# Optimization experiments

Hardware: AMD Instinct MI355X
Metric: run time of the kernel (lower is better)

The kernel has to match this reference:

```python
import jax, jax.numpy as jnp
import numpy as np

IN_CH, OUT_CH, MODES = 64, 64, 16
BATCH, N = 64, 8192


def setup_inputs() -> dict:
    key = jax.random.key(0)
    k1, k2, k3 = jax.random.split(key, 3)
    scale = 1.0 / (IN_CH * OUT_CH)
    x = jax.random.normal(k1, (BATCH, IN_CH, N), dtype=jnp.float32)
    w_real = scale * jax.random.uniform(k2, (IN_CH, OUT_CH, MODES), dtype=jnp.float32)
    w_imag = scale * jax.random.uniform(k3, (IN_CH, OUT_CH, MODES), dtype=jnp.float32)
    return {"x": x, "w_real": w_real, "w_imag": w_imag}


def reference(x, w_real, w_imag):
    # x: (b, in_ch, n) real. weights: (in_ch, out_ch, modes) complex.
    n = x.shape[-1]
    weights = w_real + 1j * w_imag                      # complex64
    x_ft = jnp.fft.rfft(x)                              # (b, in_ch, n//2+1) complex
    # multiply only the lowest `modes` frequencies by learned complex weights
    out_modes = jnp.einsum('bix,iox->box', x_ft[:, :, :MODES], weights)
    n_freq = n // 2 + 1
    out_ft = jnp.zeros((x.shape[0], OUT_CH, n_freq), dtype=jnp.complex64)
    out_ft = out_ft.at[:, :, :MODES].set(out_modes)
    return jnp.fft.irfft(out_ft, n=n)                   # (b, out_ch, n) real
```

## Files before the change

kernel.cpp:

```cpp
#include <hip/hip_runtime.h>

#define NPTS 8192

typedef __bf16 bf16x8 __attribute__((ext_vector_type(8)));
typedef short short8 __attribute__((ext_vector_type(8)));
typedef float f32x4 __attribute__((ext_vector_type(4)));


__device__ __forceinline__ void split8(const float* v, short8& h, short8& l) {
#pragma unroll
    for (int j = 0; j < 8; ++j) {
        unsigned u = __float_as_uint(v[j]);
        h[j] = (short)(u >> 16);
        float lo = v[j] - __uint_as_float(u & 0xffff0000u);
        unsigned ul = __float_as_uint(lo);
        l[j] = (short)((ul + 0x7fffu + ((ul >> 16) & 1u)) >> 16);
    }
}

__global__ __launch_bounds__(256) void prep_kernel(const float* __restrict__ wr,
                                                   const float* __restrict__ wi,
                                                   float* __restrict__ wtr,
                                                   float* __restrict__ wti,
                                                   ushort* __restrict__ bas) {
    const int bid = blockIdx.x, t = threadIdx.x;
    if (bid < 256) {
        int idx = bid * 256 + t;
        int i = idx >> 10, o = (idx >> 4) & 63, k = idx & 15;
        int dst = k * 4096 + i * 64 + o;
        wtr[dst] = wr[idx];
        wti[dst] = wi[idx];
    } else {
        int e = (bid - 256) * 256 + t;
        int j = e & 7;
        int lane = (e >> 3) & 63;
        int gk = (e >> 9) & 255;
        int ct = e >> 17;
        int m = lane & 15;
        int n = gk * 32 + ((lane >> 4) & 3) * 8 + j;
        int p = (m * n) & 8191;
        float a = (float)p * (1.0f / 4096.0f);
        float v = ct ? -sinpif(a) : cospif(a);
        unsigned u = __float_as_uint(v);
        unsigned hb = (u + 0x7fffu + ((u >> 16) & 1u)) >> 16;
        float hf = __uint_as_float(hb << 16);
        float lo = v - hf;
        unsigned ul = __float_as_uint(lo);
        unsigned lb = (ul + 0x7fffu + ((ul >> 16) & 1u)) >> 16;
        bas[e] = (ushort)hb;
        bas[262144 + e] = (ushort)lb;
    }
}

__global__ __launch_bounds__(256) void dft_kernel(const float* __restrict__ x,
                                                  const ushort* __restrict__ bas,
                                                  float* __restrict__ Xp) {
    const int t = threadIdx.x;
    const int lane = t & 63, w = t >> 6;
    const int rb = blockIdx.x >> 4, seg = blockIdx.x & 15;
    const int rowq = lane >> 4;
    const int row = rb * 64 + w * 16 + (lane & 15);
    const float* xp = x + (size_t)row * NPTS + seg * 512 + rowq * 8;
    const bf16x8* bh = (const bf16x8*)bas;
    const bf16x8* bl = (const bf16x8*)(bas + 262144);
    const int gk0 = seg * 16;

    f32x4 acc0 = {0.f, 0.f, 0.f, 0.f};
    f32x4 acc1 = {0.f, 0.f, 0.f, 0.f};

    float4 xa = *(const float4*)xp;
    float4 xb = *(const float4*)(xp + 4);
    bf16x8 c0h = bh[gk0 * 64 + lane];
    bf16x8 c1h = bh[(256 + gk0) * 64 + lane];
    bf16x8 c0l = bl[gk0 * 64 + lane];
    bf16x8 c1l = bl[(256 + gk0) * 64 + lane];

    for (int ks = 0; ks < 16; ++ks) {
        float v[8] = {xa.x, xa.y, xa.z, xa.w, xb.x, xb.y, xb.z, xb.w};
        short8 hsv, lsv;
        split8(v, hsv, lsv);
        bf16x8 ah = __builtin_bit_cast(bf16x8, hsv);
        bf16x8 al = __builtin_bit_cast(bf16x8, lsv);

        float4 nxa, nxb;
        bf16x8 n0h, n1h, n0l, n1l;
        if (ks < 15) {
            const float* xq = xp + (ks + 1) * 32;
            nxa = *(const float4*)xq;
            nxb = *(const float4*)(xq + 4);
            int gk = gk0 + ks + 1;
            n0h = bh[gk * 64 + lane];
            n1h = bh[(256 + gk) * 64 + lane];
            n0l = bl[gk * 64 + lane];
            n1l = bl[(256 + gk) * 64 + lane];
        }

        acc0 = __builtin_amdgcn_mfma_f32_16x16x32_bf16(ah, c0h, acc0, 0, 0, 0);
        acc1 = __builtin_amdgcn_mfma_f32_16x16x32_bf16(ah, c1h, acc1, 0, 0, 0);
        acc0 = __builtin_amdgcn_mfma_f32_16x16x32_bf16(al, c0h, acc0, 0, 0, 0);
        acc1 = __builtin_amdgcn_mfma_f32_16x16x32_bf16(al, c1h, acc1, 0, 0, 0);
        acc0 = __builtin_amdgcn_mfma_f32_16x16x32_bf16(ah, c0l, acc0, 0, 0, 0);
        acc1 = __builtin_amdgcn_mfma_f32_16x16x32_bf16(ah, c1l, acc1, 0, 0, 0);

        if (ks < 15) {
            xa = nxa; xb = nxb;
            c0h = n0h; c1h = n1h; c0l = n0l; c1l = n1l;
        }
    }

    const int k = lane & 15;
    const int rbase = rb * 64 + w * 16 + rowq * 4;
    *(f32x4*)&Xp[(size_t)((seg * 16 + k) * 2 + 0) * 4096 + rbase] = acc0;
    *(f32x4*)&Xp[(size_t)((seg * 16 + k) * 2 + 1) * 4096 + rbase] = acc1;
}

__global__ __launch_bounds__(256) void mix_kernel(const float* __restrict__ Xp,
                                                  const float* __restrict__ wtr,
                                                  const float* __restrict__ wti,
                                                  float* __restrict__ yc) {
    __shared__ float xre[256], xim[256];
    __shared__ float wlr[4096], wli[4096];
    const int t = threadIdx.x;
    const int k = blockIdx.x & 15, bq = blockIdx.x >> 4;
    {
        int row = bq * 256 + t;
        float re = 0.f, im = 0.f;
#pragma unroll
        for (int s = 0; s < 16; ++s) {
            re += Xp[((s * 16 + k) * 2 + 0) * 4096 + row];
            im += Xp[((s * 16 + k) * 2 + 1) * 4096 + row];
        }
        xre[t] = re;
        xim[t] = im;
#pragma unroll
        for (int j = 0; j < 4; ++j) {
            ((float4*)wlr)[t + j * 256] = ((const float4*)(wtr + k * 4096))[t + j * 256];
            ((float4*)wli)[t + j * 256] = ((const float4*)(wti + k * 4096))[t + j * 256];
        }
    }
    __syncthreads();
    const int bt = t >> 6;
    const int o = t & 63;
    float accr = 0.f, acci = 0.f;
#pragma unroll 8
    for (int i = 0; i < 64; ++i) {
        float xr = xre[bt * 64 + i], xi = xim[bt * 64 + i];
        float wr = wlr[i * 64 + o], wi = wli[i * 64 + o];
        accr += xr * wr - xi * wi;
        acci += xr * wi + xi * wr;
    }
    const float invn = 1.0f / 8192.0f;
    int row2 = (bq * 4 + bt) * 64 + o;
    if (k == 0) {
        yc[row2 * 32]      = accr * invn;
        yc[row2 * 32 + 16] = 0.f;
    } else {
        yc[row2 * 32 + k]      = 2.f * accr * invn;
        yc[row2 * 32 + 16 + k] = -2.f * acci * invn;
    }
}

__global__ __launch_bounds__(256) void synth_kernel(const float* __restrict__ yc,
                                                    float* __restrict__ out) {
    const int t = threadIdx.x;
    const int lane = t & 63, w = t >> 6;
    const int rg = blockIdx.x >> 2, nq = blockIdx.x & 3;
    const int rowbase = rg * 16;
    const int col = lane & 15;
    const int q = lane >> 4;
    const int fb = (q & 1) * 8;
    const bool isSin = q >= 2;

    bf16x8 bhf, blf;
    {
        float v[8];
        const float* cp = yc + (rowbase + col) * 32 + q * 8;
        *(float4*)&v[0] = *(const float4*)cp;
        *(float4*)&v[4] = *(const float4*)(cp + 4);
        short8 h, l;
        split8(v, h, l);
        bhf = __builtin_bit_cast(bf16x8, h);
        blf = __builtin_bit_cast(bf16x8, l);
    }

    float val[8], aux[8], cd[8], sd[8];
    const int nbase = nq * 2048 + w * 512;
    {
        int n = nbase + col;
#pragma unroll
        for (int j = 0; j < 8; ++j) {
            int fj = fb + j;
            float a = (float)((fj * n) & 8191) * (1.0f / 4096.0f);
            float c = cospif(a), s = sinpif(a);
            val[j] = isSin ? s : c;
            aux[j] = isSin ? -c : s;
            float b = (float)fj * (1.0f / 256.0f);
            cd[j] = cospif(b);
            sd[j] = sinpif(b);
        }
    }

    float* op = out + (size_t)(rowbase + col) * NPTS + nbase + q * 4;
#pragma unroll 4
    for (int it = 0; it < 32; ++it) {
        short8 h, l;
        split8(val, h, l);
        bf16x8 ah = __builtin_bit_cast(bf16x8, h);
        bf16x8 al = __builtin_bit_cast(bf16x8, l);
        f32x4 acc = {0.f, 0.f, 0.f, 0.f};
        acc = __builtin_amdgcn_mfma_f32_16x16x32_bf16(ah, bhf, acc, 0, 0, 0);
        acc = __builtin_amdgcn_mfma_f32_16x16x32_bf16(al, bhf, acc, 0, 0, 0);
        acc = __builtin_amdgcn_mfma_f32_16x16x32_bf16(ah, blf, acc, 0, 0, 0);
        *(f32x4*)(op + it * 16) = acc;
#pragma unroll
        for (int j = 0; j < 8; ++j) {
            float nv = val[j] * cd[j] - aux[j] * sd[j];
            float na = aux[j] * cd[j] + val[j] * sd[j];
            val[j] = nv;
            aux[j] = na;
        }
    }
}

extern "C" void kernel_launch(void* const* d_in, const int* in_sizes, int n_in,
                              void* d_out, int out_size, void* d_ws, size_t ws_size,
                              hipStream_t stream) {
    const float* x  = (const float*)d_in[0];
    const float* wr = (const float*)d_in[1];
    const float* wi = (const float*)d_in[2];
    float* out = (float*)d_out;
    float* ws  = (float*)d_ws;
    float* yc  = ws;
    float* wtr = ws + 131072;
    float* wti = ws + 196608;
    float* Xp  = out;
    ushort* bas = (ushort*)(out + 2097152);

    prep_kernel<<<1280, 256, 0, stream>>>(wr, wi, wtr, wti, bas);
    dft_kernel<<<1024, 256, 0, stream>>>(x, bas, Xp);
    mix_kernel<<<256, 256, 0, stream>>>(Xp, wtr, wti, yc);
    synth_kernel<<<1024, 256, 0, stream>>>(yc, out);
}
```

Measured before the change: 258.3 us.

## Fuse four kernels into one cooperative persistent kernel with grid syncs

Replaces the prep, DFT, mix and synthesis launches with a single cooperative kernel of 512 blocks that loops over two virtual blocks per stage and separates stages with grid.sync(). The goal is to remove the per-kernel launch overhead and the gaps between dependent launches. In exchange, occupancy is capped at 512 resident blocks. Each grid barrier costs something, and the mix stage leaves half of the blocks idle.

```diff
diff --git a/kernel.cpp b/kernel.cpp
--- a/kernel.cpp
+++ b/kernel.cpp
@@ -1,4 +1,7 @@
 #include <hip/hip_runtime.h>
+#include <hip/hip_cooperative_groups.h>
+
+namespace cg = cooperative_groups;
 
 #define NPTS 8192
 
@@ -18,206 +21,223 @@
     }
 }
 
-__global__ __launch_bounds__(256) void prep_kernel(const float* __restrict__ wr,
-                                                   const float* __restrict__ wi,
-                                                   float* __restrict__ wtr,
-                                                   float* __restrict__ wti,
-                                                   ushort* __restrict__ bas) {
-    const int bid = blockIdx.x, t = threadIdx.x;
-    if (bid < 256) {
-        int idx = bid * 256 + t;
-        int i = idx >> 10, o = (idx >> 4) & 63, k = idx & 15;
-        int dst = k * 4096 + i * 64 + o;
-        wtr[dst] = wr[idx];
-        wti[dst] = wi[idx];
-    } else {
-        int e = (bid - 256) * 256 + t;
-        int j = e & 7;
-        int lane = (e >> 3) & 63;
-        int gk = (e >> 9) & 255;
-        int ct = e >> 17;
-        int m = lane & 15;
-        int n = gk * 32 + ((lane >> 4) & 3) * 8 + j;
-        int p = (m * n) & 8191;
-        float a = (float)p * (1.0f / 4096.0f);
-        float v = ct ? -sinpif(a) : cospif(a);
-        unsigned u = __float_as_uint(v);
-        unsigned hb = (u + 0x7fffu + ((u >> 16) & 1u)) >> 16;
-        float hf = __uint_as_float(hb << 16);
-        float lo = v - hf;
-        unsigned ul = __float_as_uint(lo);
-        unsigned lb = (ul + 0x7fffu + ((ul >> 16) & 1u)) >> 16;
-        bas[e] = (ushort)hb;
-        bas[262144 + e] = (ushort)lb;
-    }
-}
-
-__global__ __launch_bounds__(256) void dft_kernel(const float* __restrict__ x,
-                                                  const ushort* __restrict__ bas,
-                                                  float* __restrict__ Xp) {
-    const int t = threadIdx.x;
-    const int lane = t & 63, w = t >> 6;
-    const int rb = blockIdx.x >> 4, seg = blockIdx.x & 15;
-    const int rowq = lane >> 4;
-    const int row = rb * 64 + w * 16 + (lane & 15);
-    const float* xp = x + (size_t)row * NPTS + seg * 512 + rowq * 8;
-    const bf16x8* bh = (const bf16x8*)bas;
-    const bf16x8* bl = (const bf16x8*)(bas + 262144);
-    const int gk0 = seg * 16;
-
-    f32x4 acc0 = {0.f, 0.f, 0.f, 0.f};
-    f32x4 acc1 = {0.f, 0.f, 0.f, 0.f};
-
-    float4 xa = *(const float4*)xp;
-    float4 xb = *(const float4*)(xp + 4);
-    bf16x8 c0h = bh[gk0 * 64 + lane];
-    bf16x8 c1h = bh[(256 + gk0) * 64 + lane];
-    bf16x8 c0l = bl[gk0 * 64 + lane];
-    bf16x8 c1l = bl[(256 + gk0) * 64 + lane];
-
-    for (int ks = 0; ks < 16; ++ks) {
-        float v[8] = {xa.x, xa.y, xa.z, xa.w, xb.x, xb.y, xb.z, xb.w};
-        short8 hsv, lsv;
-        split8(v, hsv, lsv);
-        bf16x8 ah = __builtin_bit_cast(bf16x8, hsv);
-        bf16x8 al = __builtin_bit_cast(bf16x8, lsv);
-
-        float4 nxa, nxb;
-        bf16x8 n0h, n1h, n0l, n1l;
-        if (ks < 15) {
-            const float* xq = xp + (ks + 1) * 32;
-            nxa = *(const float4*)xq;
-            nxb = *(const float4*)(xq + 4);
-            int gk = gk0 + ks + 1;
-            n0h = bh[gk * 64 + lane];
-            n1h = bh[(256 + gk) * 64 + lane];
-            n0l = bl[gk * 64 + lane];
-            n1l = bl[(256 + gk) * 64 + lane];
-        }
-
-        acc0 = __builtin_amdgcn_mfma_f32_16x16x32_bf16(ah, c0h, acc0, 0, 0, 0);
-        acc1 = __builtin_amdgcn_mfma_f32_16x16x32_bf16(ah, c1h, acc1, 0, 0, 0);
-        acc0 = __builtin_amdgcn_mfma_f32_16x16x32_bf16(al, c0h, acc0, 0, 0, 0);
-        acc1 = __builtin_amdgcn_mfma_f32_16x16x32_bf16(al, c1h, acc1, 0, 0, 0);
-        acc0 = __builtin_amdgcn_mfma_f32_16x16x32_bf16(ah, c0l, acc0, 0, 0, 0);
-        acc1 = __builtin_amdgcn_mfma_f32_16x16x32_bf16(ah, c1l, acc1, 0, 0, 0);
-
-        if (ks < 15) {
-            xa = nxa; xb = nxb;
-            c0h = n0h; c1h = n1h; c0l = n0l; c1l = n1l;
-        }
-    }
-
-    const int k = lane & 15;
-    const int rbase = rb * 64 + w * 16 + rowq * 4;
-    *(f32x4*)&Xp[(size_t)((seg * 16 + k) * 2 + 0) * 4096 + rbase] = acc0;
-    *(f32x4*)&Xp[(size_t)((seg * 16 + k) * 2 + 1) * 4096 + rbase] = acc1;
-}
-
-__global__ __launch_bounds__(256) void mix_kernel(const float* __restrict__ Xp,
-                                                  const float* __restrict__ wtr,
-                                                  const float* __restrict__ wti,
-                                                  float* __restrict__ yc) {
-    __shared__ float xre[256], xim[256];
-    __shared__ float wlr[4096], wli[4096];
-    const int t = threadIdx.x;
-    const int k = blockIdx.x & 15, bq = blockIdx.x >> 4;
-    {
-        int row = bq * 256 + t;
-        float re = 0.f, im = 0.f;
-#pragma unroll
-        for (int s = 0; s < 16; ++s) {
-            re += Xp[((s * 16 + k) * 2 + 0) * 4096 + row];
-            im += Xp[((s * 16 + k) * 2 + 1) * 4096 + row];
-        }
-        xre[t] = re;
-        xim[t] = im;
-#pragma unroll
-        for (int j = 0; j < 4; ++j) {
-            ((float4*)wlr)[t + j * 256] = ((const float4*)(wtr + k * 4096))[t + j * 256];
-            ((float4*)wli)[t + j * 256] = ((const float4*)(wti + k * 4096))[t + j * 256];
-        }
-    }
-    __syncthreads();
-    const int bt = t >> 6;
-    const int o = t & 63;
-    float accr = 0.f, acci = 0.f;
+__global__ __launch_bounds__(256, 2) void fused_kernel(const float* __restrict__ x,
+                                                       const float* __restrict__ wr,
+                                                       const float* __restrict__ wi,
+                                                       float* out,
+                                                       float* ws) {
+    cg::grid_group grid = cg::this_grid();
+    const int t = threadIdx.x, bid = blockIdx.x;
+    float* yc  = ws;
+    float* wtr = ws + 131072;
+    float* wti = ws + 196608;
+    float* Xp  = out;
+    ushort* bas = (ushort*)(out + 2097152);
+
+    {
+        int tid = bid * 256 + t;
+        if (tid < 65536) {
+            int i = tid >> 10, o = (tid >> 4) & 63, k = tid & 15;
+            int dst = k * 4096 + i * 64 + o;
+            wtr[dst] = wr[tid];
+            wti[dst] = wi[tid];
+        }
+#pragma unroll
+        for (int rep = 0; rep < 2; ++rep) {
+            int e = tid + rep * 131072;
+            int j = e & 7;
+            int lane = (e >> 3) & 63;
+            int gk = (e >> 9) & 255;
+            int ct = e >> 17;
+            int m = lane & 15;
+            int n = gk * 32 + ((lane >> 4) & 3) * 8 + j;
+            int p = (m * n) & 8191;
+            float a = (float)p * (1.0f / 4096.0f);
+            float v = ct ? -sinpif(a) : cospif(a);
+            unsigned u = __float_as_uint(v);
+            unsigned hb = (u + 0x7fffu + ((u >> 16) & 1u)) >> 16;
+            float hf = __uint_as_float(hb << 16);
+            float lo = v - hf;
+            unsigned ul = __float_as_uint(lo);
+            unsigned lb = (ul + 0x7fffu + ((ul >> 16) & 1u)) >> 16;
+            bas[e] = (ushort)hb;
+            bas[262144 + e] = (ushort)lb;
+        }
+    }
+    grid.sync();
+
+    {
+        const int lane = t & 63, w = t >> 6;
+        const bf16x8* bh = (const bf16x8*)bas;
+        const bf16x8* bl = (const bf16x8*)(bas + 262144);
+#pragma unroll 1
+        for (int it = 0; it < 2; ++it) {
+            const int vt = bid * 2 + it;
+            const int rb = vt >> 4, seg = vt & 15;
+            const int rowq = lane >> 4;
+            const int row = rb * 64 + w * 16 + (lane & 15);
+            const float* xp = x + (size_t)row * NPTS + seg * 512 + rowq * 8;
+            const int gk0 = seg * 16;
+
+            f32x4 acc0 = {0.f, 0.f, 0.f, 0.f};
+            f32x4 acc1 = {0.f, 0.f, 0.f, 0.f};
+
+            float4 xa = *(const float4*)xp;
+            float4 xb = *(const float4*)(xp + 4);
+            bf16x8 c0h = bh[gk0 * 64 + lane];
+            bf16x8 c1h = bh[(256 + gk0) * 64 + lane];
+            bf16x8 c0l = bl[gk0 * 64 + lane];
+            bf16x8 c1l = bl[(256 + gk0) * 64 + lane];
+
+            for (int ks = 0; ks < 16; ++ks) {
+                float v[8];
+                v[0] = xa.x; v[1] = xa.y; v[2] = xa.z; v[3] = xa.w;
+                v[4] = xb.x; v[5] = xb.y; v[6] = xb.z; v[7] = xb.w;
+                short8 hsv, lsv;
+                split8(v, hsv, lsv);
+                bf16x8 ah = __builtin_bit_cast(bf16x8, hsv);
+                bf16x8 al = __builtin_bit_cast(bf16x8, lsv);
+
+                float4 nxa, nxb;
+                bf16x8 n0h, n1h, n0l, n1l;
+                if (ks < 15) {
+                    const float* xq = xp + (ks + 1) * 32;
+                    nxa = *(const float4*)xq;
+                    nxb = *(const float4*)(xq + 4);
+                    int gk = gk0 + ks + 1;
+                    n0h = bh[gk * 64 + lane];
+                    n1h = bh[(256 + gk) * 64 + lane];
+                    n0l = bl[gk * 64 + lane];
+                    n1l = bl[(256 + gk) * 64 + lane];
+                }
+
+                acc0 = __builtin_amdgcn_mfma_f32_16x16x32_bf16(ah, c0h, acc0, 0, 0, 0);
+                acc1 = __builtin_amdgcn_mfma_f32_16x16x32_bf16(ah, c1h, acc1, 0, 0, 0);
+                acc0 = __builtin_amdgcn_mfma_f32_16x16x32_bf16(al, c0h, acc0, 0, 0, 0);
+                acc1 = __builtin_amdgcn_mfma_f32_16x16x32_bf16(al, c1h, acc1, 0, 0, 0);
+                acc0 = __builtin_amdgcn_mfma_f32_16x16x32_bf16(ah, c0l, acc0, 0, 0, 0);
+                acc1 = __builtin_amdgcn_mfma_f32_16x16x32_bf16(ah, c1l, acc1, 0, 0, 0);
+
+                if (ks < 15) {
+                    xa = nxa; xb = nxb;
+                    c0h = n0h; c1h = n1h; c0l = n0l; c1l = n1l;
+                }
+            }
+
+            const int k = lane & 15;
+            const int rbase = rb * 64 + w * 16 + rowq * 4;
+            *(f32x4*)&Xp[(size_t)((seg * 16 + k) * 2 + 0) * 4096 + rbase] = acc0;
+            *(f32x4*)&Xp[(size_t)((seg * 16 + k) * 2 + 1) * 4096 + rbase] = acc1;
+        }
+    }
+    grid.sync();
+
+    {
+        __shared__ float xre[256], xim[256];
+        __shared__ float wlr[4096], wli[4096];
+        if (bid < 256) {
+            const int k = bid & 15, bq = bid >> 4;
+            {
+                int row = bq * 256 + t;
+                float re = 0.f, im = 0.f;
+#pragma unroll
+                for (int s = 0; s < 16; ++s) {
+                    re += Xp[((s * 16 + k) * 2 + 0) * 4096 + row];
+                    im += Xp[((s * 16 + k) * 2 + 1) * 4096 + row];
+                }
+                xre[t] = re;
+                xim[t] = im;
+#pragma unroll
+                for (int j = 0; j < 4; ++j) {
+                    ((float4*)wlr)[t + j * 256] = ((const float4*)(wtr + k * 4096))[t + j * 256];
+                    ((float4*)wli)[t + j * 256] = ((const float4*)(wti + k * 4096))[t + j * 256];
+                }
+            }
+            __syncthreads();
+            const int bt = t >> 6;
+            const int o = t & 63;
+            float accr = 0.f, acci = 0.f;
 #pragma unroll 8
-    for (int i = 0; i < 64; ++i) {
-        float xr = xre[bt * 64 + i], xi = xim[bt * 64 + i];
-        float wr = wlr[i * 64 + o], wi = wli[i * 64 + o];
-        accr += xr * wr - xi * wi;
-        acci += xr * wi + xi * wr;
-    }
-    const float invn = 1.0f / 8192.0f;
-    int row2 = (bq * 4 + bt) * 64 + o;
-    if (k == 0) {
-        yc[row2 * 32]      = accr * invn;
-        yc[row2 * 32 + 16] = 0.f;
-    } else {
-        yc[row2 * 32 + k]      = 2.f * accr * invn;
-        yc[row2 * 32 + 16 + k] = -2.f * acci * invn;
-    }
-}
-
-__global__ __launch_bounds__(256) void synth_kernel(const float* __restrict__ yc,
-                                                    float* __restrict__ out) {
-    const int t = threadIdx.x;
-    const int lane = t & 63, w = t >> 6;
-    const int rg = blockIdx.x >> 2, nq = blockIdx.x & 3;
-    const int rowbase = rg * 16;
-    const int col = lane & 15;
-    const int q = lane >> 4;
-    const int fb = (q & 1) * 8;
-    const bool isSin = q >= 2;
-
-    bf16x8 bhf, blf;
-    {
-        float v[8];
-        const float* cp = yc + (rowbase + col) * 32 + q * 8;
-        *(float4*)&v[0] = *(const float4*)cp;
-        *(float4*)&v[4] = *(const float4*)(cp + 4);
-        short8 h, l;
-        split8(v, h, l);
-        bhf = __builtin_bit_cast(bf16x8, h);
-        blf = __builtin_bit_cast(bf16x8, l);
-    }
-
-    float val[8], aux[8], cd[8], sd[8];
-    const int nbase = nq * 2048 + w * 512;
-    {
-        int n = nbase + col;
-#pragma unroll
-        for (int j = 0; j < 8; ++j) {
-            int fj = fb + j;
-            float a = (float)((fj * n) & 8191) * (1.0f / 4096.0f);
-            float c = cospif(a), s = sinpif(a);
-            val[j] = isSin ? s : c;
-            aux[j] = isSin ? -c : s;
-            float b = (float)fj * (1.0f / 256.0f);
-            cd[j] = cospif(b);
-            sd[j] = sinpif(b);
-        }
-    }
-
-    float* op = out + (size_t)(rowbase + col) * NPTS + nbase + q * 4;
+            for (int i = 0; i < 64; ++i) {
+                float xr = xre[bt * 64 + i], xi = xim[bt * 64 + i];
+                float wrv = wlr[i * 64 + o], wiv = wli[i * 64 + o];
+                accr += xr * wrv - xi * wiv;
+                acci += xr * wiv + xi * wrv;
+            }
+            const float invn = 1.0f / 8192.0f;
+            int row2 = (bq * 4 + bt) * 64 + o;
+            if (k == 0) {
+                yc[row2 * 32]      = accr * invn;
+                yc[row2 * 32 + 16] = 0.f;
+            } else {
+                yc[row2 * 32 + k]      = 2.f * accr * invn;
+                yc[row2 * 32 + 16 + k] = -2.f * acci * invn;
+            }
+        }
+    }
+    grid.sync();
+
+    {
+        const int lane = t & 63, w = t >> 6;
+        const int col = lane & 15;
+        const int q = lane >> 4;
+        const int fb = (q & 1) * 8;
+        const bool isSin = q >= 2;
+#pragma unroll 1
+        for (int it2 = 0; it2 < 2; ++it2) {
+            const int vt = bid * 2 + it2;
+            const int rg = vt >> 2, nq = vt & 3;
+            const int rowbase = rg * 16;
+
+            bf16x8 bhf, blf;
+            {
+                float v[8];
+                const float* cp = yc + (rowbase + col) * 32 + q * 8;
+                *(float4*)&v[0] = *(const float4*)cp;
+                *(float4*)&v[4] = *(const float4*)(cp + 4);
+                short8 h, l;
+                split8(v, h, l);
+                bhf = __builtin_bit_cast(bf16x8, h);
+                blf = __builtin_bit_cast(bf16x8, l);
+            }
+
+            float val[8], aux[8], cd[8], sd[8];
+            const int nbase = nq * 2048 + w * 512;
+            {
+                int n = nbase + col;
+#pragma unroll
+                for (int j = 0; j < 8; ++j) {
+                    int fj = fb + j;
+                    float a = (float)((fj * n) & 8191) * (1.0f / 4096.0f);
+                    float c = cospif(a), s = sinpif(a);
+                    val[j] = isSin ? s : c;
+                    aux[j] = isSin ? -c : s;
+                    float b = (float)fj * (1.0f / 256.0f);
+                    cd[j] = cospif(b);
+                    sd[j] = sinpif(b);
+                }
+            }
+
+            float* op = out + (size_t)(rowbase + col) * NPTS + nbase + q * 4;
 #pragma unroll 4
-    for (int it = 0; it < 32; ++it) {
-        short8 h, l;
-        split8(val, h, l);
-        bf16x8 ah = __builtin_bit_cast(bf16x8, h);
-        bf16x8 al = __builtin_bit_cast(bf16x8, l);
-        f32x4 acc = {0.f, 0.f, 0.f, 0.f};
-        acc = __builtin_amdgcn_mfma_f32_16x16x32_bf16(ah, bhf, acc, 0, 0, 0);
-        acc = __builtin_amdgcn_mfma_f32_16x16x32_bf16(al, bhf, acc, 0, 0, 0);
-        acc = __builtin_amdgcn_mfma_f32_16x16x32_bf16(ah, blf, acc, 0, 0, 0);
-        *(f32x4*)(op + it * 16) = acc;
-#pragma unroll
-        for (int j = 0; j < 8; ++j) {
-            float nv = val[j] * cd[j] - aux[j] * sd[j];
-            float na = aux[j] * cd[j] + val[j] * sd[j];
-            val[j] = nv;
-            aux[j] = na;
+            for (int itn = 0; itn < 32; ++itn) {
+                short8 h, l;
+                split8(val, h, l);
+                bf16x8 ah = __builtin_bit_cast(bf16x8, h);
+                bf16x8 al = __builtin_bit_cast(bf16x8, l);
+                f32x4 acc = {0.f, 0.f, 0.f, 0.f};
+                acc = __builtin_amdgcn_mfma_f32_16x16x32_bf16(ah, bhf, acc, 0, 0, 0);
+                acc = __builtin_amdgcn_mfma_f32_16x16x32_bf16(al, bhf, acc, 0, 0, 0);
+                acc = __builtin_amdgcn_mfma_f32_16x16x32_bf16(ah, blf, acc, 0, 0, 0);
+                *(f32x4*)(op + itn * 16) = acc;
+#pragma unroll
+                for (int j = 0; j < 8; ++j) {
+                    float nv = val[j] * cd[j] - aux[j] * sd[j];
+                    float na = aux[j] * cd[j] + val[j] * sd[j];
+                    val[j] = nv;
+                    aux[j] = na;
+                }
+            }
         }
     }
 }
@@ -230,14 +250,8 @@
     const float* wi = (const float*)d_in[2];
     float* out = (float*)d_out;
     float* ws  = (float*)d_ws;
-    float* yc  = ws;
-    float* wtr = ws + 131072;
-    float* wti = ws + 196608;
-    float* Xp  = out;
-    ushort* bas = (ushort*)(out + 2097152);
-
-    prep_kernel<<<1280, 256, 0, stream>>>(wr, wi, wtr, wti, bas);
-    dft_kernel<<<1024, 256, 0, stream>>>(x, bas, Xp);
-    mix_kernel<<<256, 256, 0, stream>>>(Xp, wtr, wti, yc);
-    synth_kernel<<<1024, 256, 0, stream>>>(yc, out);
+
+    void* args[5] = {(void*)&x, (void*)&wr, (void*)&wi, (void*)&out, (void*)&ws};
+    hipLaunchCooperativeKernel((void*)fused_kernel, dim3(512), dim3(256),
+                               args, 0, stream);
 }
```

Result: slower. 459.9 us (+78.1%).
